# Kernel optimization log

Hardware: AMD Instinct MI355X
Metric: run time of the kernel (lower is better)

Reference implementation:

```python
import jax, jax.numpy as jnp
import numpy as np

B, S, IN, H = 256, 512, 512, 512

def setup_inputs() -> dict:
    key = jax.random.key(0)
    ks = jax.random.split(key, 8)
    s = 1.0 / np.sqrt(H)
    si = 1.0 / np.sqrt(IN)
    return {
        "inputs": jax.random.normal(ks[0], (B, S, IN), dtype=jnp.float32),
        "timestamps": jax.random.uniform(ks[1], (B, S), dtype=jnp.float32),
        "W_all_w": jax.random.uniform(ks[2], (4 * H, H), dtype=jnp.float32, minval=-s, maxval=s),
        "W_all_b": jax.random.uniform(ks[3], (4 * H,), dtype=jnp.float32, minval=-s, maxval=s),
        "U_all_w": jax.random.uniform(ks[4], (4 * H, IN), dtype=jnp.float32, minval=-si, maxval=si),
        "U_all_b": jax.random.uniform(ks[5], (4 * H,), dtype=jnp.float32, minval=-si, maxval=si),
        "W_d_w": jax.random.uniform(ks[6], (H, H), dtype=jnp.float32, minval=-s, maxval=s),
        "W_d_b": jax.random.uniform(ks[7], (H,), dtype=jnp.float32, minval=-s, maxval=s),
    }

def reference(inputs, timestamps, W_all_w, W_all_b, U_all_w, U_all_b, W_d_w, W_d_b):
    b, seq, _ = inputs.shape
    hsz = W_d_w.shape[0]
    # Precompute input projections for all steps at once: [B,S,4H]
    u_proj = jnp.einsum('bsi,gi->bsg', inputs, U_all_w) + U_all_b

    def step(carry, xs):
        h, c = carry
        u_t, t_t = xs  # u_t: [B,4H], t_t: [B]
        c_s1 = jnp.tanh(c @ W_d_w.T + W_d_b)
        c_adj = c - c_s1 + c_s1 * t_t[:, None]
        outs = h @ W_all_w.T + W_all_b + u_t
        f, i, o, c_tmp = jnp.split(outs, 4, axis=1)
        f = jax.nn.sigmoid(f)
        i = jax.nn.sigmoid(i)
        o = jax.nn.sigmoid(o)
        c_tmp = jnp.tanh(c_tmp)
        c = f * c_adj + i * c_tmp
        h = o * jnp.tanh(c)
        return (h, c), (o, h, c)

    h0 = jnp.zeros((b, hsz), dtype=inputs.dtype)
    c0 = jnp.zeros((b, hsz), dtype=inputs.dtype)
    (h, c), (o_seq, h_seq, c_seq) = jax.lax.scan(
        step, (h0, c0),
        (jnp.swapaxes(u_proj, 0, 1), jnp.swapaxes(timestamps, 0, 1)))
    outputs = jnp.swapaxes(o_seq, 0, 1)  # [B,S,H]
    return outputs, h, c
```

## Files before the change

kernel.cpp:

```cpp
#include <hip/hip_runtime.h>
#include <hip/hip_bf16.h>
#include <math.h>

#define BATCH 256
#define SEQ   512
#define IN_D  512
#define HID   512
#define FOURH 2048
#define BS_ROWS (BATCH * SEQ)

typedef __bf16 bf16x8 __attribute__((ext_vector_type(8)));
typedef float  f32x4  __attribute__((ext_vector_type(4)));
typedef unsigned uint32x4 __attribute__((ext_vector_type(4)));
typedef unsigned long long ull;

__device__ __forceinline__ float sigf(float x)  { return 1.0f / (1.0f + __expf(-x)); }
__device__ __forceinline__ float tanhf_(float x){ return 1.0f - 2.0f / (__expf(2.0f * x) + 1.0f); }

__global__ __launch_bounds__(256) void init_kernel(
    const float* __restrict__ W_all_w, const float* __restrict__ W_all_b,
    const float* __restrict__ U_all_w, const float* __restrict__ U_all_b,
    const float* __restrict__ W_d_w,
    __bf16* __restrict__ Wb, __bf16* __restrict__ Ub, __bf16* __restrict__ Db,
    float* __restrict__ bias_all,
    unsigned* __restrict__ hb,
    unsigned* __restrict__ cb,
    unsigned* __restrict__ bar)
{
    const int stride = gridDim.x * blockDim.x;
    const int tid0 = blockIdx.x * blockDim.x + threadIdx.x;

    const int nW = FOURH * HID;
    for (int i = tid0; i < nW; i += stride) {
        Wb[i] = (__bf16)W_all_w[i];
        Ub[i] = (__bf16)U_all_w[i];
    }
    const int nD = HID * HID;
    for (int i = tid0; i < nD; i += stride) Db[i] = (__bf16)W_d_w[i];
    for (int i = tid0; i < FOURH; i += stride) bias_all[i] = W_all_b[i] + U_all_b[i];
    for (int i = tid0; i < 2 * BATCH * 256; i += stride) { hb[i] = 0u; cb[i] = 0u; }
    for (int i = tid0; i < 16 * 2 * 32; i += stride) bar[i] = 0u;
}

__global__ __launch_bounds__(256) void uproj_gemm(
    const float* __restrict__ x, const __bf16* __restrict__ Ub,
    __bf16* __restrict__ up)
{
    const unsigned bid = blockIdx.x;
    const unsigned lg = (bid & 7) * 2048u + (bid >> 3);
    const int cb = lg & 15;
    const int rb = lg >> 4;

    __shared__ __bf16 As[128][64];
    __shared__ __bf16 Bs[128][64];

    const int tid = threadIdx.x;
    const int wave = tid >> 6, lane = tid & 63;
    const int wm = wave >> 1, wn = wave & 1;
    const int lrow = lane & 15, kq = lane >> 4;
    const int sw = (lrow & 7) << 3;

    f32x4 acc[4][4];
    #pragma unroll
    for (int m = 0; m < 4; ++m)
        #pragma unroll
        for (int n = 0; n < 4; ++n) acc[m][n] = (f32x4){0.f, 0.f, 0.f, 0.f};

    const int srow = tid >> 1;
    const int skc  = (tid & 1) * 32;
    const int dsw  = (srow & 7) << 3;

    for (int kk = 0; kk < 512; kk += 64) {
        {
            const float* xs = x + (size_t)(rb * 128 + srow) * 512 + kk + skc;
            #pragma unroll
            for (int j = 0; j < 4; ++j) {
                float4 va = ((const float4*)xs)[2 * j];
                float4 vb = ((const float4*)xs)[2 * j + 1];
                bf16x8 pk;
                pk[0] = (__bf16)va.x; pk[1] = (__bf16)va.y;
                pk[2] = (__bf16)va.z; pk[3] = (__bf16)va.w;
                pk[4] = (__bf16)vb.x; pk[5] = (__bf16)vb.y;
                pk[6] = (__bf16)vb.z; pk[7] = (__bf16)vb.w;
                *(bf16x8*)&As[srow][(skc + j * 8) ^ dsw] = pk;
            }
            const __bf16* bsrc = Ub + (size_t)(cb * 128 + srow) * 512 + kk + skc;
            #pragma unroll
            for (int j = 0; j < 4; ++j)
                *(uint4*)&Bs[srow][(skc + j * 8) ^ dsw] = *(const uint4*)(bsrc + j * 8);
        }
        __syncthreads();

        #pragma unroll
        for (int k2 = 0; k2 < 2; ++k2) {
            const int ke = k2 * 32 + kq * 8;
            bf16x8 af[4], bfr[4];
            #pragma unroll
            for (int m = 0; m < 4; ++m)
                af[m] = *(const bf16x8*)&As[wm * 64 + m * 16 + lrow][ke ^ sw];
            #pragma unroll
            for (int n = 0; n < 4; ++n)
                bfr[n] = *(const bf16x8*)&Bs[wn * 64 + n * 16 + lrow][ke ^ sw];
            #pragma unroll
            for (int m = 0; m < 4; ++m)
                #pragma unroll
                for (int n = 0; n < 4; ++n)
                    acc[m][n] = __builtin_amdgcn_mfma_f32_16x16x32_bf16(af[m], bfr[n], acc[m][n], 0, 0, 0);
        }
        __syncthreads();
    }

    const int colL = lane & 15, r0 = (lane >> 4) * 4;
    const size_t orow0 = (size_t)rb * 128 + wm * 64;
    const int ocol0 = cb * 128 + wn * 64;
    #pragma unroll
    for (int m = 0; m < 4; ++m)
        #pragma unroll
        for (int n = 0; n < 4; ++n)
            #pragma unroll
            for (int i = 0; i < 4; ++i)
                up[(orow0 + m * 16 + r0 + i) * 2048 + ocol0 + n * 16 + colL] = (__bf16)acc[m][n][i];
}

__global__ __launch_bounds__(512, 2) void scan_kernel(
    const __bf16* __restrict__ up,
    const float* __restrict__ timestamps,
    const __bf16* __restrict__ Wb,
    const __bf16* __restrict__ Db,
    const float* __restrict__ bias_all,
    const float* __restrict__ Wd_b,
    unsigned* __restrict__ hbuf,
    unsigned* __restrict__ cbuf,
    unsigned* __restrict__ bar,
    float* __restrict__ out)
{
    const int tid = threadIdx.x;
    const int bid = blockIdx.x;
    const int grp = bid & 15, blk = bid >> 4;
    const int b0 = grp * 16;
    const int k0 = blk * 32;
    const int wave = tid >> 6, lane = tid & 63;
    const int wq = wave & 3;
    const bool is_d = (wave >= 4);
    const int lrow = lane & 15, kq = lane >> 4;
    const int swz = (lrow & 7) << 3;
    const int kbase = wq * 128 + kq * 8;

    __shared__ __bf16 Ah[16][512];
    __shared__ __bf16 Ac[16][512];
    __shared__ float  exg[4][16][33][4];
    __shared__ float  exd[16][33][4];
    __shared__ __bf16 Us[2][16][128];
    __shared__ float  Ts[2][16];
    __shared__ float  Cm[512];
    __shared__ float  BiasW[128];
    __shared__ float  BiasD[32];

    bf16x8 Bg[4][2][4];
    bf16x8 Bd[2][4];
    if (!is_d) {
        #pragma unroll
        for (int u = 0; u < 4; ++u)
            #pragma unroll
            for (int ct = 0; ct < 2; ++ct)
                #pragma unroll
                for (int ks = 0; ks < 4; ++ks)
                    Bg[u][ct][ks] = *(const bf16x8*)(
                        Wb + (size_t)(u * 512 + k0 + ct * 16 + lrow) * 512 + kbase + ks * 32);
    } else {
        #pragma unroll
        for (int ct = 0; ct < 2; ++ct)
            #pragma unroll
            for (int ks = 0; ks < 4; ++ks)
                Bd[ct][ks] = *(const bf16x8*)(
                    Db + (size_t)(k0 + ct * 16 + lrow) * 512 + kbase + ks * 32);
    }

    if (tid < 128) BiasW[tid] = bias_all[(tid >> 5) * 512 + k0 + (tid & 31)];
    else if (tid < 160) BiasD[tid - 128] = Wd_b[k0 + (tid - 128)];
    Cm[tid] = 0.f;
    if (tid < 256) {
        const int row = tid >> 4, j = tid & 15, g = j >> 2, seg = j & 3;
        uint32x4 v = __builtin_nontemporal_load(
            (const uint32x4*)(up + ((size_t)(b0 + row) * 512 + 0) * 2048
                              + g * 512 + k0 + seg * 8));
        *(uint32x4*)&Us[0][row][g * 32 + seg * 8] = v;
    }
    if (tid < 16) Ts[0][tid] = timestamps[(size_t)(b0 + tid) * 512 + 0];
    __syncthreads();

    #pragma unroll 1
    for (int t = 0; t < SEQ; ++t) {
        const int par = t & 1;

        if (t > 0) {
            const unsigned* fl = &bar[(grp * 2 + par) * 32 + wq * 4];
            for (;;) {
                unsigned f = (lane < 4)
                    ? __hip_atomic_load(&fl[lane], __ATOMIC_RELAXED, __HIP_MEMORY_SCOPE_AGENT)
                    : 0xFFFFFFFFu;
                if (__all((int)(f >= (unsigned)t))) break;
                __builtin_amdgcn_s_sleep(1);
            }
        }

        {
            const ull* src = (const ull*)(is_d ? cbuf : hbuf)
                           + (size_t)par * 32768 + (size_t)b0 * 128 + wq * 32 + (lane & 31);
            ull v[8];
            #pragma unroll
            for (int l = 0; l < 8; ++l)
                v[l] = __hip_atomic_load(src + (size_t)(2 * l + (lane >> 5)) * 128,
                                         __ATOMIC_RELAXED, __HIP_MEMORY_SCOPE_AGENT);
            __bf16 (* __restrict__ dst)[512] = is_d ? Ac : Ah;
            #pragma unroll
            for (int l = 0; l < 8; ++l) {
                const int row = 2 * l + (lane >> 5);
                const int e = (wq * 128 + (lane & 31) * 4) ^ ((row & 7) << 3);
                *(ull*)&dst[row][e] = v[l];
            }
        }
        asm volatile("s_waitcnt lgkmcnt(0)" ::: "memory");
        __builtin_amdgcn_sched_barrier(0);

        const bool do_pf = (t + 1 < SEQ);
        if (!is_d) {
            f32x4 acc[4][2];
            #pragma unroll
            for (int u = 0; u < 4; ++u)
                #pragma unroll
                for (int ct = 0; ct < 2; ++ct) acc[u][ct] = (f32x4){0.f, 0.f, 0.f, 0.f};
            #pragma unroll
            for (int ks = 0; ks < 4; ++ks) {
                bf16x8 a = *(const bf16x8*)&Ah[lrow][(kbase + ks * 32) ^ swz];
                #pragma unroll
                for (int u = 0; u < 4; ++u)
                    #pragma unroll
                    for (int ct = 0; ct < 2; ++ct)
                        acc[u][ct] = __builtin_amdgcn_mfma_f32_16x16x32_bf16(
                            a, Bg[u][ct][ks], acc[u][ct], 0, 0, 0);
            }
            const int colL = lane & 15;
            #pragma unroll
            for (int u = 0; u < 4; ++u)
                #pragma unroll
                for (int ct = 0; ct < 2; ++ct)
                    #pragma unroll
                    for (int i = 0; i < 4; ++i)
                        exg[u][kq * 4 + i][ct * 16 + colL][wq] = acc[u][ct][i];
        } else {
            uint32x4 upf;
            float tpf = 0.f;
            const int tid2 = tid - 256;
            if (do_pf) {
                const int row = tid2 >> 4, j = tid2 & 15, g = j >> 2, seg = j & 3;
                upf = __builtin_nontemporal_load(
                    (const uint32x4*)(up + ((size_t)(b0 + row) * 512 + (t + 1)) * 2048
                                      + g * 512 + k0 + seg * 8));
                if (tid2 < 16) tpf = timestamps[(size_t)(b0 + tid2) * 512 + (t + 1)];
            }

            f32x4 accd[2];
            accd[0] = (f32x4){0.f, 0.f, 0.f, 0.f};
            accd[1] = (f32x4){0.f, 0.f, 0.f, 0.f};
            #pragma unroll
            for (int ks = 0; ks < 4; ++ks) {
                bf16x8 a = *(const bf16x8*)&Ac[lrow][(kbase + ks * 32) ^ swz];
                #pragma unroll
                for (int ct = 0; ct < 2; ++ct)
                    accd[ct] = __builtin_amdgcn_mfma_f32_16x16x32_bf16(
                        a, Bd[ct][ks], accd[ct], 0, 0, 0);
            }
            const int colL = lane & 15;
            #pragma unroll
            for (int ct = 0; ct < 2; ++ct)
                #pragma unroll
                for (int i = 0; i < 4; ++i)
                    exd[kq * 4 + i][ct * 16 + colL][wq] = accd[ct][i];

            if (do_pf) {
                const int row = tid2 >> 4, j = tid2 & 15, g = j >> 2, seg = j & 3;
                *(uint32x4*)&Us[par ^ 1][row][g * 32 + seg * 8] = upf;
                if (tid2 < 16) Ts[par ^ 1][tid2] = tpf;
            }
        }
        __syncthreads();

        float o_def = 0.f;
        {
            const int r = tid >> 5, kcol = tid & 31;
            f32x4 pd = *(const f32x4*)&exd[r][kcol][0];
            float g4[4];
            #pragma unroll
            for (int g = 0; g < 4; ++g) {
                f32x4 p = *(const f32x4*)&exg[g][r][kcol][0];
                g4[g] = BiasW[g * 32 + kcol] + (float)Us[par][r][g * 32 + kcol]
                      + (p[0] + p[1]) + (p[2] + p[3]);
            }
            const float dd = BiasD[kcol] + (pd[0] + pd[1]) + (pd[2] + pd[3]);

            const float c_old = Cm[tid];
            const float tt = Ts[par][r];
            const float c_s1  = tanhf_(dd);
            const float c_adj = c_old - c_s1 + c_s1 * tt;
            const float f  = sigf(g4[0]);
            const float ii = sigf(g4[1]);
            const float o  = sigf(g4[2]);
            const float c_tmp = tanhf_(g4[3]);
            const float c_new = f * c_adj + ii * c_tmp;
            const float h_new = o * tanhf_(c_new);
            Cm[tid] = c_new;

            if (t == SEQ - 1) {
                __builtin_nontemporal_store(o,
                    &out[((size_t)(b0 + r) * 512 + t) * 512 + k0 + kcol]);
                const size_t base = (size_t)BATCH * SEQ * HID;
                out[base + (size_t)(b0 + r) * 512 + k0 + kcol] = h_new;
                out[base + (size_t)BATCH * HID + (size_t)(b0 + r) * 512 + k0 + kcol] = c_new;
            } else {
                o_def = o;
                const unsigned hb16 = (unsigned)__builtin_bit_cast(unsigned short, (__bf16)h_new);
                const unsigned cb16 = (unsigned)__builtin_bit_cast(unsigned short, (__bf16)c_new);
                const unsigned hn = (unsigned)__shfl_xor((int)hb16, 1);
                const unsigned cn = (unsigned)__shfl_xor((int)cb16, 1);
                if (!(lane & 1)) {
                    const unsigned hp = hb16 | (hn << 16);
                    const unsigned cp = cb16 | (cn << 16);
                    const size_t e = (size_t)(par ^ 1) * 65536
                                   + (size_t)(b0 + r) * 256 + ((k0 + kcol) >> 1);
                    __hip_atomic_store(hbuf + e, hp, __ATOMIC_RELAXED, __HIP_MEMORY_SCOPE_AGENT);
                    __hip_atomic_store(cbuf + e, cp, __ATOMIC_RELAXED, __HIP_MEMORY_SCOPE_AGENT);
                }
            }
        }
        __syncthreads();

        if (t < SEQ - 1) {
            if (tid == 0)
                __hip_atomic_store(&bar[(grp * 2 + ((t + 1) & 1)) * 32 + blk],
                                   (unsigned)(t + 1),
                                   __ATOMIC_RELAXED, __HIP_MEMORY_SCOPE_AGENT);
            {
                const int r = tid >> 5, kcol = tid & 31;
                __builtin_nontemporal_store(o_def,
                    &out[((size_t)(b0 + r) * 512 + t) * 512 + k0 + kcol]);
            }
        }
    }
}

extern "C" void kernel_launch(void* const* d_in, const int* in_sizes, int n_in,
                              void* d_out, int out_size, void* d_ws, size_t ws_size,
                              hipStream_t stream) {
    const float* inputs     = (const float*)d_in[0];
    const float* timestamps = (const float*)d_in[1];
    const float* W_all_w    = (const float*)d_in[2];
    const float* W_all_b    = (const float*)d_in[3];
    const float* U_all_w    = (const float*)d_in[4];
    const float* U_all_b    = (const float*)d_in[5];
    const float* W_d_w      = (const float*)d_in[6];
    const float* W_d_b      = (const float*)d_in[7];
    float* out = (float*)d_out;

    char* ws = (char*)d_ws;
    size_t off = 0;
    auto alloc = [&](size_t bytes) -> void* {
        void* p = ws + off;
        off += (bytes + 255) & ~(size_t)255;
        return p;
    };
    __bf16* Wb       = (__bf16*)alloc((size_t)FOURH * HID * 2);
    __bf16* Ub       = (__bf16*)alloc((size_t)FOURH * HID * 2);
    __bf16* Db       = (__bf16*)alloc((size_t)HID * HID * 2);
    float*  bias_all = (float*) alloc((size_t)FOURH * 4);
    unsigned* hbuf   = (unsigned*)alloc((size_t)2 * BATCH * 256 * 4);
    unsigned* cbuf   = (unsigned*)alloc((size_t)2 * BATCH * 256 * 4);
    unsigned* bar    = (unsigned*)alloc(16 * 2 * 32 * 4);
    __bf16* up       = (__bf16*)alloc((size_t)BS_ROWS * FOURH * 2);

    hipLaunchKernelGGL(init_kernel, dim3(1024), dim3(256), 0, stream,
                       W_all_w, W_all_b, U_all_w, U_all_b, W_d_w,
                       Wb, Ub, Db, bias_all, hbuf, cbuf, bar);

    hipLaunchKernelGGL(uproj_gemm, dim3(16384), dim3(256), 0, stream,
                       inputs, Ub, up);

    void* sargs[] = {
        (void*)&up, (void*)&timestamps, (void*)&Wb, (void*)&Db,
        (void*)&bias_all, (void*)&W_d_b,
        (void*)&hbuf, (void*)&cbuf, (void*)&bar, (void*)&out
    };
    hipLaunchCooperativeKernel((const void*)scan_kernel, dim3(256), dim3(512),
                               sargs, 0, stream);
}
```

Before: 2.471 ms.

## Replace flag barrier with step-tagged h/c values and double-buffered exchange

Removes the per-group flag barrier. Each bf16 h/c value is now stored in a 32-bit word whose upper 16 bits carry the step number, and consumers poll the data itself until every tag matches. The shared-memory reduction buffers are double-buffered by parity and XOR-swizzled, which lets the second __syncthreads per step be dropped, and the prefetch of the next step's projection is issued before the spin. This cuts synchronisation round trips on the serial recurrence, but doubles the bytes exchanged through global memory and makes the polling loop reread the whole tile on every retry.

```diff
diff --git a/kernel.cpp b/kernel.cpp
--- a/kernel.cpp
+++ b/kernel.cpp
@@ -24,8 +24,7 @@
     __bf16* __restrict__ Wb, __bf16* __restrict__ Ub, __bf16* __restrict__ Db,
     float* __restrict__ bias_all,
     unsigned* __restrict__ hb,
-    unsigned* __restrict__ cb,
-    unsigned* __restrict__ bar)
+    unsigned* __restrict__ cb)
 {
     const int stride = gridDim.x * blockDim.x;
     const int tid0 = blockIdx.x * blockDim.x + threadIdx.x;
@@ -38,8 +37,7 @@
     const int nD = HID * HID;
     for (int i = tid0; i < nD; i += stride) Db[i] = (__bf16)W_d_w[i];
     for (int i = tid0; i < FOURH; i += stride) bias_all[i] = W_all_b[i] + U_all_b[i];
-    for (int i = tid0; i < 2 * BATCH * 256; i += stride) { hb[i] = 0u; cb[i] = 0u; }
-    for (int i = tid0; i < 16 * 2 * 32; i += stride) bar[i] = 0u;
+    for (int i = tid0; i < 2 * BATCH * HID; i += stride) { hb[i] = 0u; cb[i] = 0u; }
 }
 
 __global__ __launch_bounds__(256) void uproj_gemm(
@@ -131,7 +129,6 @@
     const float* __restrict__ Wd_b,
     unsigned* __restrict__ hbuf,
     unsigned* __restrict__ cbuf,
-    unsigned* __restrict__ bar,
     float* __restrict__ out)
 {
     const int tid = threadIdx.x;
@@ -148,8 +145,8 @@
 
     __shared__ __bf16 Ah[16][512];
     __shared__ __bf16 Ac[16][512];
-    __shared__ float  exg[4][16][33][4];
-    __shared__ float  exd[16][33][4];
+    __shared__ float  exg[2][4][4][16][32];
+    __shared__ float  exd[2][4][16][32];
     __shared__ __bf16 Us[2][16][128];
     __shared__ float  Ts[2][16];
     __shared__ float  Cm[512];
@@ -189,41 +186,55 @@
     if (tid < 16) Ts[0][tid] = timestamps[(size_t)(b0 + tid) * 512 + 0];
     __syncthreads();
 
+    const ull* gsrc = (const ull*)(is_d ? cbuf : hbuf);
+    const int c2 = wq * 128 + lane * 2;
+
     #pragma unroll 1
     for (int t = 0; t < SEQ; ++t) {
         const int par = t & 1;
-
-        if (t > 0) {
-            const unsigned* fl = &bar[(grp * 2 + par) * 32 + wq * 4];
-            for (;;) {
-                unsigned f = (lane < 4)
-                    ? __hip_atomic_load(&fl[lane], __ATOMIC_RELAXED, __HIP_MEMORY_SCOPE_AGENT)
-                    : 0xFFFFFFFFu;
-                if (__all((int)(f >= (unsigned)t))) break;
-                __builtin_amdgcn_s_sleep(1);
-            }
-        }
-
+        const unsigned tt = (unsigned)t;
+
+        uint32x4 upf;
+        float tpf = 0.f;
+        const bool do_pf = (t + 1 < SEQ);
+        const int tid2 = tid - 256;
+        if (is_d && do_pf) {
+            const int row = tid2 >> 4, j = tid2 & 15, g = j >> 2, seg = j & 3;
+            upf = __builtin_nontemporal_load(
+                (const uint32x4*)(up + ((size_t)(b0 + row) * 512 + (t + 1)) * 2048
+                                  + g * 512 + k0 + seg * 8));
+            if (tid2 < 16) tpf = timestamps[(size_t)(b0 + tid2) * 512 + (t + 1)];
+        }
+
+        const ull* src = gsrc + (size_t)par * 65536 + (size_t)b0 * 256 + wq * 64 + lane;
+        ull v[16];
+        for (;;) {
+            unsigned bad = 0u;
+            #pragma unroll
+            for (int l = 0; l < 16; ++l)
+                v[l] = __hip_atomic_load(src + (size_t)l * 256,
+                                         __ATOMIC_RELAXED, __HIP_MEMORY_SCOPE_AGENT);
+            #pragma unroll
+            for (int l = 0; l < 16; ++l) {
+                const unsigned lo = (unsigned)v[l], hi = (unsigned)(v[l] >> 32);
+                bad |= (lo >> 16) ^ tt;
+                bad |= (hi >> 16) ^ tt;
+            }
+            if (__all((int)(bad == 0u))) break;
+            __builtin_amdgcn_s_sleep(1);
+        }
         {
-            const ull* src = (const ull*)(is_d ? cbuf : hbuf)
-                           + (size_t)par * 32768 + (size_t)b0 * 128 + wq * 32 + (lane & 31);
-            ull v[8];
-            #pragma unroll
-            for (int l = 0; l < 8; ++l)
-                v[l] = __hip_atomic_load(src + (size_t)(2 * l + (lane >> 5)) * 128,
-                                         __ATOMIC_RELAXED, __HIP_MEMORY_SCOPE_AGENT);
             __bf16 (* __restrict__ dst)[512] = is_d ? Ac : Ah;
             #pragma unroll
-            for (int l = 0; l < 8; ++l) {
-                const int row = 2 * l + (lane >> 5);
-                const int e = (wq * 128 + (lane & 31) * 4) ^ ((row & 7) << 3);
-                *(ull*)&dst[row][e] = v[l];
+            for (int l = 0; l < 16; ++l) {
+                const unsigned lo = (unsigned)v[l], hi = (unsigned)(v[l] >> 32);
+                const unsigned pk = (lo & 0xFFFFu) | (hi << 16);
+                *(unsigned*)&dst[l][c2 ^ ((l & 7) << 3)] = pk;
             }
         }
         asm volatile("s_waitcnt lgkmcnt(0)" ::: "memory");
         __builtin_amdgcn_sched_barrier(0);
 
-        const bool do_pf = (t + 1 < SEQ);
         if (!is_d) {
             f32x4 acc[4][2];
             #pragma unroll
@@ -246,20 +257,11 @@
                 #pragma unroll
                 for (int ct = 0; ct < 2; ++ct)
                     #pragma unroll
-                    for (int i = 0; i < 4; ++i)
-                        exg[u][kq * 4 + i][ct * 16 + colL][wq] = acc[u][ct][i];
+                    for (int i = 0; i < 4; ++i) {
+                        const int row = kq * 4 + i;
+                        exg[par][wq][u][row][(ct * 16 + colL) ^ (row & 7)] = acc[u][ct][i];
+                    }
         } else {
-            uint32x4 upf;
-            float tpf = 0.f;
-            const int tid2 = tid - 256;
-            if (do_pf) {
-                const int row = tid2 >> 4, j = tid2 & 15, g = j >> 2, seg = j & 3;
-                upf = __builtin_nontemporal_load(
-                    (const uint32x4*)(up + ((size_t)(b0 + row) * 512 + (t + 1)) * 2048
-                                      + g * 512 + k0 + seg * 8));
-                if (tid2 < 16) tpf = timestamps[(size_t)(b0 + tid2) * 512 + (t + 1)];
-            }
-
             f32x4 accd[2];
             accd[0] = (f32x4){0.f, 0.f, 0.f, 0.f};
             accd[1] = (f32x4){0.f, 0.f, 0.f, 0.f};
@@ -275,34 +277,36 @@
             #pragma unroll
             for (int ct = 0; ct < 2; ++ct)
                 #pragma unroll
-                for (int i = 0; i < 4; ++i)
-                    exd[kq * 4 + i][ct * 16 + colL][wq] = accd[ct][i];
-
-            if (do_pf) {
-                const int row = tid2 >> 4, j = tid2 & 15, g = j >> 2, seg = j & 3;
-                *(uint32x4*)&Us[par ^ 1][row][g * 32 + seg * 8] = upf;
-                if (tid2 < 16) Ts[par ^ 1][tid2] = tpf;
-            }
+                for (int i = 0; i < 4; ++i) {
+                    const int row = kq * 4 + i;
+                    exd[par][wq][row][(ct * 16 + colL) ^ (row & 7)] = accd[ct][i];
+                }
         }
         __syncthreads();
 
-        float o_def = 0.f;
+        if (is_d && do_pf) {
+            const int row = tid2 >> 4, j = tid2 & 15, g = j >> 2, seg = j & 3;
+            *(uint32x4*)&Us[par ^ 1][row][g * 32 + seg * 8] = upf;
+            if (tid2 < 16) Ts[par ^ 1][tid2] = tpf;
+        }
+
         {
             const int r = tid >> 5, kcol = tid & 31;
-            f32x4 pd = *(const f32x4*)&exd[r][kcol][0];
+            const int kx = kcol ^ (r & 7);
             float g4[4];
             #pragma unroll
-            for (int g = 0; g < 4; ++g) {
-                f32x4 p = *(const f32x4*)&exg[g][r][kcol][0];
+            for (int g = 0; g < 4; ++g)
                 g4[g] = BiasW[g * 32 + kcol] + (float)Us[par][r][g * 32 + kcol]
-                      + (p[0] + p[1]) + (p[2] + p[3]);
-            }
-            const float dd = BiasD[kcol] + (pd[0] + pd[1]) + (pd[2] + pd[3]);
+                      + (exg[par][0][g][r][kx] + exg[par][1][g][r][kx])
+                      + (exg[par][2][g][r][kx] + exg[par][3][g][r][kx]);
+            const float dd = BiasD[kcol]
+                     + (exd[par][0][r][kx] + exd[par][1][r][kx])
+                     + (exd[par][2][r][kx] + exd[par][3][r][kx]);
 
             const float c_old = Cm[tid];
-            const float tt = Ts[par][r];
+            const float tsv = Ts[par][r];
             const float c_s1  = tanhf_(dd);
-            const float c_adj = c_old - c_s1 + c_s1 * tt;
+            const float c_adj = c_old - c_s1 + c_s1 * tsv;
             const float f  = sigf(g4[0]);
             const float ii = sigf(g4[1]);
             const float o  = sigf(g4[2]);
@@ -318,31 +322,14 @@
                 out[base + (size_t)(b0 + r) * 512 + k0 + kcol] = h_new;
                 out[base + (size_t)BATCH * HID + (size_t)(b0 + r) * 512 + k0 + kcol] = c_new;
             } else {
-                o_def = o;
-                const unsigned hb16 = (unsigned)__builtin_bit_cast(unsigned short, (__bf16)h_new);
-                const unsigned cb16 = (unsigned)__builtin_bit_cast(unsigned short, (__bf16)c_new);
-                const unsigned hn = (unsigned)__shfl_xor((int)hb16, 1);
-                const unsigned cn = (unsigned)__shfl_xor((int)cb16, 1);
-                if (!(lane & 1)) {
-                    const unsigned hp = hb16 | (hn << 16);
-                    const unsigned cp = cb16 | (cn << 16);
-                    const size_t e = (size_t)(par ^ 1) * 65536
-                                   + (size_t)(b0 + r) * 256 + ((k0 + kcol) >> 1);
-                    __hip_atomic_store(hbuf + e, hp, __ATOMIC_RELAXED, __HIP_MEMORY_SCOPE_AGENT);
-                    __hip_atomic_store(cbuf + e, cp, __ATOMIC_RELAXED, __HIP_MEMORY_SCOPE_AGENT);
-                }
-            }
-        }
-        __syncthreads();
-
-        if (t < SEQ - 1) {
-            if (tid == 0)
-                __hip_atomic_store(&bar[(grp * 2 + ((t + 1) & 1)) * 32 + blk],
-                                   (unsigned)(t + 1),
-                                   __ATOMIC_RELAXED, __HIP_MEMORY_SCOPE_AGENT);
-            {
-                const int r = tid >> 5, kcol = tid & 31;
-                __builtin_nontemporal_store(o_def,
+                const unsigned tag = ((unsigned)(t + 1)) << 16;
+                const unsigned hw = (unsigned)__builtin_bit_cast(unsigned short, (__bf16)h_new) | tag;
+                const unsigned cw = (unsigned)__builtin_bit_cast(unsigned short, (__bf16)c_new) | tag;
+                const size_t e = (size_t)(par ^ 1) * 131072
+                               + (size_t)(b0 + r) * 512 + k0 + kcol;
+                __hip_atomic_store(hbuf + e, hw, __ATOMIC_RELAXED, __HIP_MEMORY_SCOPE_AGENT);
+                __hip_atomic_store(cbuf + e, cw, __ATOMIC_RELAXED, __HIP_MEMORY_SCOPE_AGENT);
+                __builtin_nontemporal_store(o,
                     &out[((size_t)(b0 + r) * 512 + t) * 512 + k0 + kcol]);
             }
         }
@@ -373,14 +360,13 @@
     __bf16* Ub       = (__bf16*)alloc((size_t)FOURH * HID * 2);
     __bf16* Db       = (__bf16*)alloc((size_t)HID * HID * 2);
     float*  bias_all = (float*) alloc((size_t)FOURH * 4);
-    unsigned* hbuf   = (unsigned*)alloc((size_t)2 * BATCH * 256 * 4);
-    unsigned* cbuf   = (unsigned*)alloc((size_t)2 * BATCH * 256 * 4);
-    unsigned* bar    = (unsigned*)alloc(16 * 2 * 32 * 4);
+    unsigned* hbuf   = (unsigned*)alloc((size_t)2 * BATCH * HID * 4);
+    unsigned* cbuf   = (unsigned*)alloc((size_t)2 * BATCH * HID * 4);
     __bf16* up       = (__bf16*)alloc((size_t)BS_ROWS * FOURH * 2);
 
     hipLaunchKernelGGL(init_kernel, dim3(1024), dim3(256), 0, stream,
                        W_all_w, W_all_b, U_all_w, U_all_b, W_d_w,
-                       Wb, Ub, Db, bias_all, hbuf, cbuf, bar);
+                       Wb, Ub, Db, bias_all, hbuf, cbuf);
 
     hipLaunchKernelGGL(uproj_gemm, dim3(16384), dim3(256), 0, stream,
                        inputs, Ub, up);
@@ -388,7 +374,7 @@
     void* sargs[] = {
         (void*)&up, (void*)&timestamps, (void*)&Wb, (void*)&Db,
         (void*)&bias_all, (void*)&W_d_b,
-        (void*)&hbuf, (void*)&cbuf, (void*)&bar, (void*)&out
+        (void*)&hbuf, (void*)&cbuf, (void*)&out
     };
     hipLaunchCooperativeKernel((const void*)scan_kernel, dim3(256), dim3(512),
                                sargs, 0, stream);
```

Result: slower. 3.591 ms (+45.4%).
